# Optimization experiments

Hardware: AMD Instinct MI355X
Metric: run time of the kernel (lower is better)

Reference implementation:

```python
import jax, jax.numpy as jnp
import numpy as np

B, N, K, IN = 8, 2048, 8, 5
BN = B * N

def _lin(k, i, o):
    s = 1.0 / np.sqrt(i)
    return jax.random.uniform(k, (i, o), jnp.float32, -s, s)

def setup_inputs() -> dict:
    key = jax.random.key(0)
    ks = jax.random.split(key, 12)
    inp = {"points": jax.random.normal(ks[0], (B, N, IN), jnp.float32)}
    dims = [(IN * 2, 64), (64 * 2, 128), (128 * 2, 256)]
    for n, (i, o) in enumerate(dims, 1):
        inp[f"W{n}"] = _lin(ks[n], i, o)
        inp[f"b{n}"] = jnp.zeros((o,), jnp.float32)
        inp[f"g{n}"] = jnp.ones((o,), jnp.float32)
        inp[f"be{n}"] = jnp.zeros((o,), jnp.float32)
    inp["Wf1"] = _lin(ks[10], 448, 512); inp["bf1"] = jnp.zeros((512,), jnp.float32)
    inp["gf"] = jnp.ones((512,), jnp.float32); inp["bef"] = jnp.zeros((512,), jnp.float32)
    inp["Wf2"] = _lin(ks[11], 512, 128); inp["bf2"] = jnp.zeros((128,), jnp.float32)
    return inp

def _lrelu(x):
    return jnp.where(x >= 0, x, 0.2 * x)

def _bn(x, g, b, eps=1e-5):
    # BatchNorm1d in training mode: per-feature batch statistics
    m = x.mean(0)
    v = x.var(0)
    return (x - m) * jax.lax.rsqrt(v + eps) * g + b

def _knn_idx(pos):
    # pos: [B,N,3] -> neighbor indices [B,N,K], self excluded
    sq = (pos * pos).sum(-1)
    d = sq[:, :, None] + sq[:, None, :] - 2.0 * jnp.einsum('bnc,bmc->bnm', pos, pos)
    d = d + jnp.eye(N, dtype=d.dtype) * 1e10  # exclude self
    _, idx = jax.lax.top_k(-d, K)
    return idx

def _edge_conv(x, src, dst, W, b, g, be):
    # PyG EdgeConv: msg = nn(cat[x_i, x_j - x_i]); aggr='max' at target i
    xc = x[dst]
    xn = x[src]
    h = jnp.concatenate([xc, xn - xc], axis=-1) @ W + b
    h = _bn(_lrelu(h), g, be)
    return jax.ops.segment_max(h, dst, num_segments=BN)

def reference(points, W1, b1, g1, be1, W2, b2, g2, be2, W3, b3, g3, be3,
              Wf1, bf1, gf, bef, Wf2, bf2):
    pos = points[..., :3]                      # [B,N,3]
    idx = _knn_idx(pos)                        # [B,N,K]
    offs = (jnp.arange(B) * N)[:, None, None]
    src = (idx + offs).reshape(-1)             # neighbor (source) node ids [E]
    dst = jnp.repeat(jnp.arange(BN), K)        # center (target) node ids [E]
    x = points.reshape(BN, IN)
    x1 = _edge_conv(x, src, dst, W1, b1, g1, be1)   # [BN,64]
    x2 = _edge_conv(x1, src, dst, W2, b2, g2, be2)  # [BN,128]
    x3 = _edge_conv(x2, src, dst, W3, b3, g3, be3)  # [BN,256]
    xs = jnp.concatenate([x1, x2, x3], axis=-1).reshape(B, N, 448)
    gfeat = xs.max(axis=1)                     # global max pool per cloud [B,448]
    h = _bn(_lrelu(gfeat @ Wf1 + bf1), gf, bef)
    return h @ Wf2 + bf2                       # [B,128]
```

## Files before the change

### kernel.cpp

```cpp
#include <hip/hip_runtime.h>
#include <math.h>

#define B_ 8
#define N_ 2048
#define K_ 8
#define IN_ 5
#define BN_ (B_*N_)
#define NEDGE_ (BN_*K_)
#define GRP 8
#define SEG_ 32
#define CSEG_ (N_/SEG_)
#define CHUNKS_ (N_/GRP)

typedef unsigned short ushort8_ __attribute__((ext_vector_type(8)));
typedef short bf16x8_ __attribute__((ext_vector_type(8)));
typedef float f32x4_ __attribute__((ext_vector_type(4)));

__device__ inline unsigned short f2bf(float f) {
    unsigned int u = __float_as_uint(f);
    u += 0x7fffu + ((u >> 16) & 1u);
    return (unsigned short)(u >> 16);
}
__device__ inline float bf2f(unsigned short h) {
    return __uint_as_float(((unsigned int)h) << 16);
}

__device__ inline unsigned int ord_f32(float f) {
    unsigned int u = __float_as_uint(f);
    return (u & 0x80000000u) ? ~u : (u | 0x80000000u);
}

__global__ __launch_bounds__(256) void knn_part(const float* __restrict__ points,
                                                unsigned long long* __restrict__ part) {
    int tid = threadIdx.x;
    int q = blockIdx.x * 256 + tid;
    int b = q / N_;
    int n = q % N_;
    int seg = blockIdx.y;
    const float* pb = points + (size_t)b * N_ * IN_;

    __shared__ float4 sp4[CSEG_];
    if (tid < CSEG_) {
        int j = seg * CSEG_ + tid;
        float x = pb[(size_t)j*IN_+0], y = pb[(size_t)j*IN_+1], z = pb[(size_t)j*IN_+2];
        sp4[tid] = make_float4(x, y, z, x*x + y*y + z*z);
    }
    float qx = pb[(size_t)n*IN_+0], qy = pb[(size_t)n*IN_+1], qz = pb[(size_t)n*IN_+2];
    float qsq = qx*qx + qy*qy + qz*qz;
    __syncthreads();

    unsigned long long best[K_];
#pragma unroll
    for (int k = 0; k < K_; ++k) best[k] = ~0ull;

    auto ins = [&](unsigned long long cur) {
#pragma unroll
        for (int p = 0; p < K_; ++p) {
            unsigned long long lo = best[p] < cur ? best[p] : cur;
            unsigned long long hi = best[p] < cur ? cur : best[p];
            best[p] = lo; cur = hi;
        }
    };

    int jbase = seg * CSEG_;
    for (int jj = 0; jj < CSEG_; jj += 2) {
        float4 c0 = sp4[jj], c1 = sp4[jj+1];
        float d0 = qsq + c0.w - 2.0f*(qx*c0.x + qy*c0.y + qz*c0.z);
        float d1 = qsq + c1.w - 2.0f*(qx*c1.x + qy*c1.y + qz*c1.z);
        int j0 = jbase + jj, j1 = j0 + 1;
        unsigned long long k0 = ((unsigned long long)ord_f32(d0) << 32) | (unsigned int)j0;
        unsigned long long k1 = ((unsigned long long)ord_f32(d1) << 32) | (unsigned int)j1;
        if (j0 == n) k0 = ~0ull;
        if (j1 == n) k1 = ~0ull;
        unsigned long long kmin = k0 < k1 ? k0 : k1;
        if (kmin < best[K_-1]) {
            if (k0 < best[K_-1]) ins(k0);
            if (k1 < best[K_-1]) ins(k1);
        }
    }
    unsigned long long* op = part + ((size_t)seg * BN_ + q) * K_;
#pragma unroll
    for (int k = 0; k < K_; ++k) op[k] = best[k];
}

__global__ __launch_bounds__(128) void knn_merge(const unsigned long long* __restrict__ part,
                                                 int* __restrict__ src) {
    int q = blockIdx.x * 128 + threadIdx.x;
    int b = q / N_;
    unsigned long long best[K_];
#pragma unroll
    for (int k = 0; k < K_; ++k) best[k] = ~0ull;
    for (int s = 0; s < SEG_; ++s) {
        const unsigned long long* lp = part + ((size_t)s * BN_ + q) * K_;
#pragma unroll
        for (int k = 0; k < K_; ++k) {
            unsigned long long key = lp[k];
            if (key >= best[K_-1]) break;
            unsigned long long cur = key;
#pragma unroll
            for (int p = 0; p < K_; ++p) {
                unsigned long long lo = best[p] < cur ? best[p] : cur;
                unsigned long long hi = best[p] < cur ? cur : best[p];
                best[p] = lo; cur = hi;
            }
        }
    }
#pragma unroll
    for (int k = 0; k < K_; ++k)
        src[(size_t)q*K_ + k] = b*N_ + (int)(best[k] & 0xFFFFFFFFu);
}

__global__ __launch_bounds__(256) void cast_split(const float* __restrict__ X,
                                                  unsigned short* __restrict__ Xh,
                                                  unsigned short* __restrict__ Xl,
                                                  int Kin, int Kpad, int total8) {
    int t = blockIdx.x * 256 + threadIdx.x;
    if (t >= total8) return;
    int vpr = Kpad >> 3;
    int m = t / vpr;
    int k0 = (t % vpr) * 8;
    ushort8_ vh, vl;
#pragma unroll
    for (int j = 0; j < 8; ++j) {
        int k = k0 + j;
        float v = (k < Kin) ? X[(size_t)m*Kin + k] : 0.0f;
        unsigned short h = f2bf(v);
        vh[j] = h;
        vl[j] = f2bf(v - bf2f(h));
    }
    *(ushort8_*)(Xh + (size_t)m*Kpad + k0) = vh;
    *(ushort8_*)(Xl + (size_t)m*Kpad + k0) = vl;
}

__global__ __launch_bounds__(256) void prep_layer(const float* __restrict__ W,
                                                  const float* __restrict__ scale,
                                                  const float* __restrict__ shift,
                                                  const float* __restrict__ bias,
                                                  unsigned short* __restrict__ WTh,
                                                  unsigned short* __restrict__ WTl,
                                                  float* __restrict__ cvec,
                                                  int Cin, int C, int Kpad) {
    int idx = blockIdx.x * 256 + threadIdx.x;
    int nWT = 2*C*Kpad;
    if (idx < nWT) {
        int n = idx / Kpad;
        int k = idx % Kpad;
        float val = 0.0f;
        if (k < Cin) {
            float s = scale ? scale[k] : 1.0f;
            if (n < C) val = s * (W[(size_t)k*C + n] - W[(size_t)(Cin+k)*C + n]);
            else       val = s * W[(size_t)(Cin+k)*C + (n - C)];
        }
        unsigned short h = f2bf(val);
        WTh[(size_t)n*Kpad + k] = h;
        WTl[(size_t)n*Kpad + k] = f2bf(val - bf2f(h));
    } else if (idx < nWT + C) {
        int c = idx - nWT;
        float acc = bias[c];
        if (shift)
            for (int d = 0; d < Cin; ++d) acc += shift[d] * W[(size_t)d*C + c];
        cvec[c] = acc;
    }
}

__global__ __launch_bounds__(256) void mfma_dual(const unsigned short* __restrict__ Xh,
                                                 const unsigned short* __restrict__ Xl,
                                                 const unsigned short* __restrict__ WTh,
                                                 const unsigned short* __restrict__ WTl,
                                                 float* __restrict__ PQ, int K, int Ntot) {
    __shared__ unsigned short sXh[128*32], sXl[128*32], sWh[128*32], sWl[128*32];
    int tid = threadIdx.x, l = tid & 63, w = tid >> 6;
    int wr = w >> 1, wc = w & 1;
    int bm = blockIdx.y * 128, bn0 = blockIdx.x * 128;

    f32x4_ acc[4][4];
#pragma unroll
    for (int i = 0; i < 4; ++i)
#pragma unroll
        for (int j = 0; j < 4; ++j) acc[i][j] = (f32x4_){0.f, 0.f, 0.f, 0.f};

    for (int k0 = 0; k0 < K; k0 += 32) {
#pragma unroll
        for (int i = 0; i < 2; ++i) {
            int idx = tid + i*256;
            int row = idx >> 2;
            int col0 = (idx & 3) * 8;
            size_t gx = (size_t)(bm  + row)*K + k0 + col0;
            size_t gw = (size_t)(bn0 + row)*K + k0 + col0;
            int lo_ = ((row << 6) | (col0 << 1)) ^ ((row & 7) << 4);
            *(ushort8_*)((char*)sXh + lo_) = *(const ushort8_*)(Xh + gx);
            *(ushort8_*)((char*)sXl + lo_) = *(const ushort8_*)(Xl + gx);
            *(ushort8_*)((char*)sWh + lo_) = *(const ushort8_*)(WTh + gw);
            *(ushort8_*)((char*)sWl + lo_) = *(const ushort8_*)(WTl + gw);
        }
        __syncthreads();

        int kb = (l >> 4) << 4;
        bf16x8_ bh[4], bl4[4];
#pragma unroll
        for (int nf = 0; nf < 4; ++nf) {
            int rn = wc*64 + nf*16 + (l & 15);
            int o = ((rn << 6) | kb) ^ ((rn & 7) << 4);
            bh[nf]  = *(const bf16x8_*)((const char*)sWh + o);
            bl4[nf] = *(const bf16x8_*)((const char*)sWl + o);
        }
#pragma unroll
        for (int mf = 0; mf < 4; ++mf) {
            int rm = wr*64 + mf*16 + (l & 15);
            int o = ((rm << 6) | kb) ^ ((rm & 7) << 4);
            bf16x8_ ah = *(const bf16x8_*)((const char*)sXh + o);
            bf16x8_ al = *(const bf16x8_*)((const char*)sXl + o);
#pragma unroll
            for (int nf = 0; nf < 4; ++nf) {
                acc[mf][nf] = __builtin_amdgcn_mfma_f32_16x16x32_bf16(ah, bh[nf],  acc[mf][nf], 0, 0, 0);
                acc[mf][nf] = __builtin_amdgcn_mfma_f32_16x16x32_bf16(ah, bl4[nf], acc[mf][nf], 0, 0, 0);
                acc[mf][nf] = __builtin_amdgcn_mfma_f32_16x16x32_bf16(al, bh[nf],  acc[mf][nf], 0, 0, 0);
            }
        }
        __syncthreads();
    }

    int r0 = (l >> 4) << 2, cB = l & 15;
#pragma unroll
    for (int mf = 0; mf < 4; ++mf)
#pragma unroll
        for (int nf = 0; nf < 4; ++nf) {
            int col = bn0 + wc*64 + nf*16 + cB;
#pragma unroll
            for (int reg = 0; reg < 4; ++reg) {
                int row = bm + wr*64 + mf*16 + r0 + reg;
                PQ[(size_t)row*Ntot + col] = acc[mf][nf][reg];
            }
        }
}

__global__ void combine_kernel(const float* __restrict__ P, const float* __restrict__ Q,
                               const float* __restrict__ cvec, const int* __restrict__ src,
                               unsigned short* __restrict__ Xh_out, unsigned short* __restrict__ Xl_out,
                               float* __restrict__ partial, float* __restrict__ gpart,
                               int C, int S) {
    int c = threadIdx.x;
    int i0 = blockIdx.x * GRP;
    float cv = cvec[c];
    float sum = 0.f, ssq = 0.f;
    float bmx = -INFINITY;
    for (int g = 0; g < GRP; ++g) {
        int i = i0 + g;
        float p = P[(size_t)i*S + c] + cv;
        float mx = -INFINITY;
#pragma unroll
        for (int k = 0; k < K_; ++k) {
            int s = src[(size_t)i*K_ + k];
            float h = p + Q[(size_t)s*S + c];
            float l = (h >= 0.f) ? h : 0.2f*h;
            sum += l; ssq += l*l;
            mx = fmaxf(mx, l);
        }
        if (Xh_out) {
            unsigned short hh = f2bf(mx);
            Xh_out[(size_t)i*C + c] = hh;
            Xl_out[(size_t)i*C + c] = f2bf(mx - bf2f(hh));
        }
        bmx = fmaxf(bmx, mx);
    }
    gpart[(size_t)blockIdx.x*C + c] = bmx;
    partial[(size_t)blockIdx.x*2*C + c]     = sum;
    partial[(size_t)blockIdx.x*2*C + C + c] = ssq;
}

__global__ __launch_bounds__(256) void reduce_kernel(const float* __restrict__ partial, int nblocks, int C,
                              const float* __restrict__ g, const float* __restrict__ be,
                              float* __restrict__ scale, float* __restrict__ shift) {
    int c = blockIdx.x;
    float s0 = 0.f, s1 = 0.f;
    for (int blk = threadIdx.x; blk < nblocks; blk += 256) {
        s0 += partial[(size_t)blk*2*C + c];
        s1 += partial[(size_t)blk*2*C + C + c];
    }
    __shared__ float l0[256], l1[256];
    l0[threadIdx.x] = s0; l1[threadIdx.x] = s1;
    __syncthreads();
    for (int off = 128; off > 0; off >>= 1) {
        if (threadIdx.x < off) {
            l0[threadIdx.x] += l0[threadIdx.x + off];
            l1[threadIdx.x] += l1[threadIdx.x + off];
        }
        __syncthreads();
    }
    if (threadIdx.x == 0) {
        float mean = l0[0] / (float)NEDGE_;
        float var  = l1[0] / (float)NEDGE_ - mean*mean;
        float sc = g[c] * rsqrtf(var + 1e-5f);
        scale[c] = sc;
        shift[c] = be[c] - mean*sc;
    }
}

__global__ __launch_bounds__(1024) void gmax_finalize(
        const float* __restrict__ gp1, const float* __restrict__ gp2, const float* __restrict__ gp3,
        const float* __restrict__ sc1, const float* __restrict__ sh1,
        const float* __restrict__ sc2, const float* __restrict__ sh2,
        const float* __restrict__ sc3, const float* __restrict__ sh3,
        float* __restrict__ gfeat) {
    int b = blockIdx.x, grp = blockIdx.y;
    const float *gp, *sc, *sh; int C, c0, coff;
    if (grp == 0)      { gp = gp1; sc = sc1; sh = sh1; C = 64;  c0 = 0;            coff = 0;   }
    else if (grp <= 2) { gp = gp2; sc = sc2; sh = sh2; C = 128; c0 = (grp-1)*64;   coff = 64;  }
    else               { gp = gp3; sc = sc3; sh = sh3; C = 256; c0 = (grp-3)*64;   coff = 192; }
    int cl = threadIdx.x & 63;
    int stripe = threadIdx.x >> 6;
    int c = c0 + cl;
    float mx = -INFINITY;
    for (int ch = stripe; ch < CHUNKS_; ch += 16)
        mx = fmaxf(mx, gp[((size_t)b*CHUNKS_ + ch)*C + c]);
    __shared__ float red[16][64];
    red[stripe][cl] = mx;
    __syncthreads();
    for (int off = 8; off > 0; off >>= 1) {
        if (stripe < off) red[stripe][cl] = fmaxf(red[stripe][cl], red[stripe+off][cl]);
        __syncthreads();
    }
    if (stripe == 0)
        gfeat[b*448 + coff + c] = sc[c]*red[0][cl] + sh[c];
}

__global__ __launch_bounds__(256) void final1(const float* __restrict__ gfeat,
                                              const float* __restrict__ Wf1, const float* __restrict__ bf1,
                                              const float* __restrict__ gf, const float* __restrict__ bef,
                                              float* __restrict__ H) {
    __shared__ float gfs[B_][448];
    __shared__ float red[4][64][B_];
    int t = threadIdx.x;
    int cl = t & 63;
    int stripe = t >> 6;
    int c = blockIdx.x * 64 + cl;
    for (int e = t; e < B_*448; e += 256) gfs[e/448][e%448] = gfeat[e];
    __syncthreads();
    float acc[B_] = {};
    for (int d = stripe*112; d < stripe*112 + 112; ++d) {
        float w = Wf1[(size_t)d*512 + c];
#pragma unroll
        for (int r = 0; r < B_; ++r) acc[r] += gfs[r][d] * w;
    }
#pragma unroll
    for (int r = 0; r < B_; ++r) red[stripe][cl][r] = acc[r];
    __syncthreads();
    if (stripe == 0) {
        float v[B_];
        float b1v = bf1[c];
#pragma unroll
        for (int r = 0; r < B_; ++r) {
            float a = red[0][cl][r] + red[1][cl][r] + red[2][cl][r] + red[3][cl][r] + b1v;
            v[r] = (a >= 0.f) ? a : 0.2f*a;
        }
        float mean = 0.f;
#pragma unroll
        for (int r = 0; r < B_; ++r) mean += v[r];
        mean *= (1.0f/B_);
        float var = 0.f;
#pragma unroll
        for (int r = 0; r < B_; ++r) { float dd = v[r] - mean; var += dd*dd; }
        var *= (1.0f/B_);
        float sc = gf[c] * rsqrtf(var + 1e-5f);
        float sh = bef[c] - mean*sc;
#pragma unroll
        for (int r = 0; r < B_; ++r) H[(size_t)r*512 + c] = v[r]*sc + sh;
    }
}

__global__ __launch_bounds__(128) void final2(const float* __restrict__ H,
                                              const float* __restrict__ Wf2, const float* __restrict__ bf2,
                                              float* __restrict__ out) {
    int b = blockIdx.x, c = threadIdx.x;
    __shared__ float hs[512];
    for (int e = c; e < 512; e += 128) hs[e] = H[(size_t)b*512 + e];
    __syncthreads();
    float a = bf2[c];
    for (int d = 0; d < 512; ++d) a += hs[d] * Wf2[(size_t)d*128 + c];
    out[b*128 + c] = a;
}

static void run_layer(int Kpad, int C,
                      const float* W, const float* g, const float* be, const float* b,
                      const float* scale_in, const float* shift_in,
                      float* PQ, const unsigned short* Xh_in, const unsigned short* Xl_in,
                      unsigned short* Xh_next, unsigned short* Xl_next,
                      unsigned short* WTh, unsigned short* WTl, float* cvec,
                      const int* src, float* partial, float* gpart,
                      float* scale_out, float* shift_out, hipStream_t stream) {
    int Cin = (scale_in == nullptr) ? IN_ : Kpad;
    int nPrep = 2*C*Kpad + C;
    prep_layer<<<(nPrep + 255)/256, 256, 0, stream>>>(W, scale_in, shift_in, b, WTh, WTl, cvec, Cin, C, Kpad);
    mfma_dual<<<dim3(2*C/128, BN_/128), 256, 0, stream>>>(Xh_in, Xl_in, WTh, WTl, PQ, Kpad, 2*C);
    combine_kernel<<<BN_/GRP, C, 0, stream>>>(PQ, PQ + C, cvec, src, Xh_next, Xl_next, partial, gpart, C, 2*C);
    reduce_kernel<<<C, 256, 0, stream>>>(partial, BN_/GRP, C, g, be, scale_out, shift_out);
}

extern "C" void kernel_launch(void* const* d_in, const int* in_sizes, int n_in,
                              void* d_out, int out_size, void* d_ws, size_t ws_size,
                              hipStream_t stream) {
    (void)in_sizes; (void)n_in; (void)out_size; (void)ws_size;
    const float* points = (const float*)d_in[0];
    const float* W1 = (const float*)d_in[1];  const float* b1 = (const float*)d_in[2];
    const float* g1 = (const float*)d_in[3];  const float* be1 = (const float*)d_in[4];
    const float* W2 = (const float*)d_in[5];  const float* b2 = (const float*)d_in[6];
    const float* g2 = (const float*)d_in[7];  const float* be2 = (const float*)d_in[8];
    const float* W3 = (const float*)d_in[9];  const float* b3 = (const float*)d_in[10];
    const float* g3 = (const float*)d_in[11]; const float* be3 = (const float*)d_in[12];
    const float* Wf1 = (const float*)d_in[13]; const float* bf1 = (const float*)d_in[14];
    const float* gf = (const float*)d_in[15];  const float* bef = (const float*)d_in[16];
    const float* Wf2 = (const float*)d_in[17]; const float* bf2 = (const float*)d_in[18];
    float* out = (float*)d_out;

    size_t off = 0;
    char* base = (char*)d_ws;
    auto carve = [&](size_t bytes) -> void* {
        void* p = base + off;
        off += (bytes + 255) & ~(size_t)255;
        return p;
    };
    int*   src     = (int*)  carve((size_t)NEDGE_ * 4);
    float* PQ      = (float*)carve((size_t)BN_ * 512 * 4);
    float* gp1     = (float*)carve((size_t)(BN_/GRP) * 64 * 4);
    float* gp2     = (float*)carve((size_t)(BN_/GRP) * 128 * 4);
    float* gp3     = (float*)carve((size_t)(BN_/GRP) * 256 * 4);
    unsigned short* XhA = (unsigned short*)carve((size_t)BN_ * 128 * 2);
    unsigned short* XlA = (unsigned short*)carve((size_t)BN_ * 128 * 2);
    unsigned short* XhB = (unsigned short*)carve((size_t)BN_ * 128 * 2);
    unsigned short* XlB = (unsigned short*)carve((size_t)BN_ * 128 * 2);
    unsigned short* WTh = (unsigned short*)carve((size_t)512 * 128 * 2);
    unsigned short* WTl = (unsigned short*)carve((size_t)512 * 128 * 2);
    float* cvec    = (float*)carve(256 * 4);
    float* sc1     = (float*)carve(64 * 4);
    float* sh1     = (float*)carve(64 * 4);
    float* sc2     = (float*)carve(128 * 4);
    float* sh2     = (float*)carve(128 * 4);
    float* sc3     = (float*)carve(256 * 4);
    float* sh3     = (float*)carve(256 * 4);
    float* partial = (float*)carve((size_t)(BN_/GRP) * 2 * 256 * 4);
    float* gfeat   = (float*)carve((size_t)B_ * 448 * 4);
    float* H       = (float*)carve((size_t)B_ * 512 * 4);

    unsigned long long* part = (unsigned long long*)PQ;
    knn_part<<<dim3(BN_/256, SEG_), 256, 0, stream>>>(points, part);
    knn_merge<<<BN_/128, 128, 0, stream>>>(part, src);

    int total8 = BN_ * 32 / 8;
    cast_split<<<(total8 + 255)/256, 256, 0, stream>>>(points, XhA, XlA, IN_, 32, total8);

    run_layer(32, 64,  W1, g1, be1, b1, nullptr, nullptr,
              PQ, XhA, XlA, XhB, XlB, WTh, WTl, cvec, src, partial, gp1, sc1, sh1, stream);
    run_layer(64, 128, W2, g2, be2, b2, sc1, sh1,
              PQ, XhB, XlB, XhA, XlA, WTh, WTl, cvec, src, partial, gp2, sc2, sh2, stream);
    run_layer(128, 256, W3, g3, be3, b3, sc2, sh2,
              PQ, XhA, XlA, nullptr, nullptr, WTh, WTl, cvec, src, partial, gp3, sc3, sh3, stream);

    gmax_finalize<<<dim3(B_, 7), 1024, 0, stream>>>(gp1, gp2, gp3,
                                                    sc1, sh1, sc2, sh2, sc3, sh3, gfeat);

    final1<<<8, 256, 0, stream>>>(gfeat, Wf1, bf1, gf, bef, H);
    final2<<<8, 128, 0, stream>>>(H, Wf2, bf2, out);
}
```

Measured before the change: 255.7 us.

## Precompute packed float4 points for kNN and remap combine block order

```diff
diff --git a/kernel.cpp b/kernel.cpp
--- a/kernel.cpp
+++ b/kernel.cpp
@@ -30,52 +30,43 @@
     return (u & 0x80000000u) ? ~u : (u | 0x80000000u);
 }
 
-__global__ __launch_bounds__(256) void knn_part(const float* __restrict__ points,
+__global__ __launch_bounds__(256) void knn_part(const float4* __restrict__ P4,
                                                 unsigned long long* __restrict__ part) {
     int tid = threadIdx.x;
     int q = blockIdx.x * 256 + tid;
-    int b = q / N_;
-    int n = q % N_;
+    int b = q >> 11;
+    int nloc = q & (N_-1);
     int seg = blockIdx.y;
-    const float* pb = points + (size_t)b * N_ * IN_;
-
-    __shared__ float4 sp4[CSEG_];
-    if (tid < CSEG_) {
-        int j = seg * CSEG_ + tid;
-        float x = pb[(size_t)j*IN_+0], y = pb[(size_t)j*IN_+1], z = pb[(size_t)j*IN_+2];
-        sp4[tid] = make_float4(x, y, z, x*x + y*y + z*z);
-    }
-    float qx = pb[(size_t)n*IN_+0], qy = pb[(size_t)n*IN_+1], qz = pb[(size_t)n*IN_+2];
-    float qsq = qx*qx + qy*qy + qz*qz;
-    __syncthreads();
+
+    float4 qp = P4[q];
+    float qx2 = -2.0f*qp.x, qy2 = -2.0f*qp.y, qz2 = -2.0f*qp.z;
+    float qsq = qp.w;
 
     unsigned long long best[K_];
 #pragma unroll
     for (int k = 0; k < K_; ++k) best[k] = ~0ull;
 
-    auto ins = [&](unsigned long long cur) {
-#pragma unroll
-        for (int p = 0; p < K_; ++p) {
-            unsigned long long lo = best[p] < cur ? best[p] : cur;
-            unsigned long long hi = best[p] < cur ? cur : best[p];
-            best[p] = lo; cur = hi;
-        }
-    };
-
+    const float4* __restrict__ cb = P4 + (size_t)b*N_ + (size_t)seg*CSEG_;
     int jbase = seg * CSEG_;
-    for (int jj = 0; jj < CSEG_; jj += 2) {
-        float4 c0 = sp4[jj], c1 = sp4[jj+1];
-        float d0 = qsq + c0.w - 2.0f*(qx*c0.x + qy*c0.y + qz*c0.z);
-        float d1 = qsq + c1.w - 2.0f*(qx*c1.x + qy*c1.y + qz*c1.z);
-        int j0 = jbase + jj, j1 = j0 + 1;
-        unsigned long long k0 = ((unsigned long long)ord_f32(d0) << 32) | (unsigned int)j0;
-        unsigned long long k1 = ((unsigned long long)ord_f32(d1) << 32) | (unsigned int)j1;
-        if (j0 == n) k0 = ~0ull;
-        if (j1 == n) k1 = ~0ull;
-        unsigned long long kmin = k0 < k1 ? k0 : k1;
-        if (kmin < best[K_-1]) {
-            if (k0 < best[K_-1]) ins(k0);
-            if (k1 < best[K_-1]) ins(k1);
+
+#pragma unroll 8
+    for (int jj = 0; jj < CSEG_; ++jj) {
+        float4 c = cb[jj];
+        float d = qsq + c.w;
+        d = fmaf(qx2, c.x, d);
+        d = fmaf(qy2, c.y, d);
+        d = fmaf(qz2, c.z, d);
+        int jg = jbase + jj;
+        d = (jg == nloc) ? INFINITY : d;
+        unsigned long long key = ((unsigned long long)ord_f32(d) << 32) | (unsigned int)jg;
+        if (key < best[K_-1]) {
+            unsigned long long cur = key;
+#pragma unroll
+            for (int p = 0; p < K_; ++p) {
+                unsigned long long lo = best[p] < cur ? best[p] : cur;
+                unsigned long long hi = best[p] < cur ? cur : best[p];
+                best[p] = lo; cur = hi;
+            }
         }
     }
     unsigned long long* op = part + ((size_t)seg * BN_ + q) * K_;
@@ -113,23 +104,30 @@
 __global__ __launch_bounds__(256) void cast_split(const float* __restrict__ X,
                                                   unsigned short* __restrict__ Xh,
                                                   unsigned short* __restrict__ Xl,
+                                                  float4* __restrict__ P4,
                                                   int Kin, int Kpad, int total8) {
     int t = blockIdx.x * 256 + threadIdx.x;
-    if (t >= total8) return;
-    int vpr = Kpad >> 3;
-    int m = t / vpr;
-    int k0 = (t % vpr) * 8;
-    ushort8_ vh, vl;
-#pragma unroll
-    for (int j = 0; j < 8; ++j) {
-        int k = k0 + j;
-        float v = (k < Kin) ? X[(size_t)m*Kin + k] : 0.0f;
-        unsigned short h = f2bf(v);
-        vh[j] = h;
-        vl[j] = f2bf(v - bf2f(h));
-    }
-    *(ushort8_*)(Xh + (size_t)m*Kpad + k0) = vh;
-    *(ushort8_*)(Xl + (size_t)m*Kpad + k0) = vl;
+    if (t < total8) {
+        int vpr = Kpad >> 3;
+        int m = t / vpr;
+        int k0 = (t % vpr) * 8;
+        ushort8_ vh, vl;
+#pragma unroll
+        for (int j = 0; j < 8; ++j) {
+            int k = k0 + j;
+            float v = (k < Kin) ? X[(size_t)m*Kin + k] : 0.0f;
+            unsigned short h = f2bf(v);
+            vh[j] = h;
+            vl[j] = f2bf(v - bf2f(h));
+        }
+        *(ushort8_*)(Xh + (size_t)m*Kpad + k0) = vh;
+        *(ushort8_*)(Xl + (size_t)m*Kpad + k0) = vl;
+    }
+    if (t < BN_) {
+        const float* p = X + (size_t)t*Kin;
+        float x = p[0], y = p[1], z = p[2];
+        P4[t] = make_float4(x, y, z, x*x + y*y + z*z);
+    }
 }
 
 __global__ __launch_bounds__(256) void prep_layer(const float* __restrict__ W,
@@ -239,8 +237,10 @@
                                unsigned short* __restrict__ Xh_out, unsigned short* __restrict__ Xl_out,
                                float* __restrict__ partial, float* __restrict__ gpart,
                                int C, int S) {
+    int pb = blockIdx.x;
+    int lb = (pb & 7) * CHUNKS_ + (pb >> 3);
     int c = threadIdx.x;
-    int i0 = blockIdx.x * GRP;
+    int i0 = lb * GRP;
     float cv = cvec[c];
     float sum = 0.f, ssq = 0.f;
     float bmx = -INFINITY;
@@ -263,9 +263,9 @@
         }
         bmx = fmaxf(bmx, mx);
     }
-    gpart[(size_t)blockIdx.x*C + c] = bmx;
-    partial[(size_t)blockIdx.x*2*C + c]     = sum;
-    partial[(size_t)blockIdx.x*2*C + C + c] = ssq;
+    gpart[(size_t)lb*C + c] = bmx;
+    partial[(size_t)lb*2*C + c]     = sum;
+    partial[(size_t)lb*2*C + C + c] = ssq;
 }
 
 __global__ __launch_bounds__(256) void reduce_kernel(const float* __restrict__ partial, int nblocks, int C,
@@ -430,6 +430,7 @@
     unsigned short* XlB = (unsigned short*)carve((size_t)BN_ * 128 * 2);
     unsigned short* WTh = (unsigned short*)carve((size_t)512 * 128 * 2);
     unsigned short* WTl = (unsigned short*)carve((size_t)512 * 128 * 2);
+    float4* P4     = (float4*)carve((size_t)BN_ * 16);
     float* cvec    = (float*)carve(256 * 4);
     float* sc1     = (float*)carve(64 * 4);
     float* sh1     = (float*)carve(64 * 4);
@@ -441,12 +442,12 @@
     float* gfeat   = (float*)carve((size_t)B_ * 448 * 4);
     float* H       = (float*)carve((size_t)B_ * 512 * 4);
 
+    int total8 = BN_ * 32 / 8;
+    cast_split<<<(total8 + 255)/256, 256, 0, stream>>>(points, XhA, XlA, P4, IN_, 32, total8);
+
     unsigned long long* part = (unsigned long long*)PQ;
-    knn_part<<<dim3(BN_/256, SEG_), 256, 0, stream>>>(points, part);
+    knn_part<<<dim3(BN_/256, SEG_), 256, 0, stream>>>(P4, part);
     knn_merge<<<BN_/128, 128, 0, stream>>>(part, src);
-
-    int total8 = BN_ * 32 / 8;
-    cast_split<<<(total8 + 255)/256, 256, 0, stream>>>(points, XhA, XlA, IN_, 32, total8);
 
     run_layer(32, 64,  W1, g1, be1, b1, nullptr, nullptr,
               PQ, XhA, XlA, XhB, XlB, WTh, WTl, cvec, src, partial, gp1, sc1, sh1, stream);
```

Measured after the change: 251.0 us. No clear change (-1.8%).
